# Performance work log

Measured on AMD Instinct MI355X. Metric: run time of the kernel, lower is better.

## Reference

```python
import jax, jax.numpy as jnp
import numpy as np
import math

D = 256
NS = 64
KNB = 8
VOCAB = 32000
B, S = 4, 1024
NEG = -10000.0


def _normalize(x, eps=1e-12):
    n = jnp.linalg.norm(x, axis=-1, keepdims=True)
    return x / jnp.maximum(n, eps)


def _sparsemax(z):
    # sparsemax along last axis (descending sort + cumsum threshold)
    z_sorted = -jnp.sort(-z, axis=-1)
    cumsum = jnp.cumsum(z_sorted, axis=-1)
    k = jnp.arange(1, z.shape[-1] + 1, dtype=z.dtype)
    z_check = (1.0 + k * z_sorted > cumsum).astype(z.dtype)
    k_z = z_check.sum(axis=-1, keepdims=True)
    tau = (jnp.take_along_axis(cumsum, (k_z - 1).astype(jnp.int32), axis=-1) - 1.0) / k_z
    return jnp.clip(z - tau, 0.0)


def setup_inputs() -> dict:
    key = jax.random.key(0)
    ks = jax.random.split(key, 16)
    inp = {
        'messages': jax.random.normal(ks[0], (B, S, D), jnp.float32),
        'hidden': jax.random.normal(ks[1], (B, S, D), jnp.float32),
        'x_ids': jax.random.randint(ks[2], (B, S), 0, VOCAB),
        'scn': jax.random.normal(ks[3], (B, S, NS), jnp.float32),
        'mask': jax.random.bernoulli(ks[4], 0.3, (S, S)),
        'static_nb': jax.random.randint(ks[5], (VOCAB, KNB), 0, VOCAB),
        'geo_velocity': jax.random.normal(ks[6], (B, S, NS), jnp.float32),
        'ctx_conf': jax.random.uniform(ks[7], (B, S, 1), jnp.float32),
        'current_entropy': jax.random.uniform(ks[8], (B, S), jnp.float32) * math.log(VOCAB),
        # parameters (torch Linear weight layout: [out, in])
        'W_vel': jax.random.normal(ks[9], (D, NS), jnp.float32) / np.sqrt(NS),
        'W_e1': jax.random.normal(ks[10], (8, 1), jnp.float32),
        'b_e1': jax.random.normal(ks[11], (8,), jnp.float32) * 0.1,
        'W_e2': jax.random.normal(ks[12], (1, 8), jnp.float32) / np.sqrt(8),
        'b_e2': jax.random.normal(ks[13], (1,), jnp.float32) * 0.1,
        'W_probe': jax.random.normal(ks[14], (D, D), jnp.float32) / np.sqrt(D),
        'W_gate': jnp.zeros((1, D), jnp.float32),
        'b_gate': jnp.full((1,), -4.0, jnp.float32),
    }
    return inp


def reference(messages, hidden, x_ids, scn, mask, static_nb, geo_velocity,
              ctx_conf, current_entropy, W_vel, W_e1, b_e1, W_e2, b_e2,
              W_probe, W_gate, b_gate):
    Bd, Sd, Dh = messages.shape
    f32 = messages.dtype
    blocked = (mask | jnp.eye(Sd, dtype=bool))[None]  # [1,S,S] mask + diagonal

    # ---- geo branch ----
    endpoint = _normalize(scn + 0.4 * geo_velocity)
    endpoint_sim = jnp.einsum('bsn,btn->bst', endpoint, scn)
    endpoint_sim = jnp.where(blocked, NEG, endpoint_sim)
    H_norm = jax.lax.stop_gradient(current_entropy)[..., None] / (math.log(VOCAB) + 1e-8)
    vel_h = geo_velocity @ W_vel.T
    h_aimed = _normalize(hidden + 0.3 * vel_h)
    h_msg_sim = jnp.einsum('bsd,btd->bst', h_aimed, messages)
    combined_geo = (endpoint_sim * H_norm + 0.5 * h_msg_sim) * 5.0
    combined_geo = jnp.where(blocked, NEG, combined_geo)
    ew_geo = _sparsemax(combined_geo)
    geo_agg = jnp.einsum('bst,btd->bsd', ew_geo, messages)

    # ---- static neighbor-vocab branch ----
    nb_vocab = static_nb[x_ids]  # [B,S,Knb]
    match = (x_ids[:, None, None, :] == nb_vocab[..., None]).astype(f32)  # [B,S,Knb,S]
    causal = jnp.tril(jnp.ones((Sd, Sd), f32))
    match = match * causal[None, :, None, :]
    coverage = jnp.minimum(match.sum(-1), 1.0).mean(-1, keepdims=True)  # [B,S,1]
    nb_msgs_s = jnp.einsum('bskp,bpd->bskd', match, messages)
    nb_scn_s = jnp.einsum('bskp,bpn->bskn', match, scn)
    sim_s = (nb_scn_s * scn[:, :, None, :]).sum(-1)  # [B,S,Knb]
    h_e = jax.nn.gelu(sim_s[..., None] @ W_e1.T + b_e1, approximate=False)
    edge_out = (h_e @ W_e2.T + b_e2)[..., 0]  # [B,S,Knb]
    ew_s = jax.nn.softmax(edge_out, axis=-1)
    static_agg = (nb_msgs_s * ew_s[..., None]).sum(2)

    # ---- local mode branch ----
    my_mode = jnp.argmax(scn, axis=-1)
    same_mode = (my_mode[:, :, None] == my_mode[:, None, :]).astype(f32)
    same_mode = jnp.where(blocked, 0.0, same_mode)
    scn_sim = jnp.einsum('bsn,btn->bst', scn, scn) * same_mode
    has_nb = same_mode.sum(-1, keepdims=True) > 0
    pos = jnp.arange(Sd, dtype=f32)
    pos_sim = -jnp.abs(pos[:, None] - pos[None, :])[None]
    pos_sim = jnp.where(blocked, NEG, pos_sim)
    routing_sim = jnp.where(has_nb, scn_sim, pos_sim * 0.01)
    routing_sim = jnp.where(blocked, NEG, routing_sim)
    ew_l = _sparsemax(routing_sim * 5.0)
    local_agg = jnp.einsum('bst,btd->bsd', ew_l, messages)

    # ---- gated fusion ----
    static_final = coverage * static_agg + (1.0 - coverage) * local_agg
    raw_gate = jax.nn.sigmoid(hidden @ W_gate.T + b_gate)
    geo_weight = raw_gate * ctx_conf
    agg = geo_weight * geo_agg + (1.0 - geo_weight) * static_final
    probe = _normalize(hidden @ W_probe.T)
    agg_n = _normalize(agg)
    rel = jax.nn.sigmoid((agg_n * probe).sum(-1, keepdims=True))
    return agg * rel
```

## Files before the change

### kernel.cpp

```cpp
#include <hip/hip_runtime.h>
#include <math.h>

#define D_ 256
#define NS_ 64
#define KNB_ 8
#define SEQ_ 1024
#define B_ 4
#define MAXQ_ 1024
#define NEG_ (-10000.0f)
#define BLKNEG_ (-50000.0f)

#define MSGP_B 262144
#define SCNP_B 65536
#define ASTEPS 12

typedef short bf16x8 __attribute__((ext_vector_type(8)));
typedef float f32x4 __attribute__((ext_vector_type(4)));

__device__ __forceinline__ float waveSum(float v) {
#pragma unroll
    for (int off = 32; off; off >>= 1) v += __shfl_xor(v, off, 64);
    return v;
}

__device__ __forceinline__ void waveSum2(float& a, float& b) {
#pragma unroll
    for (int off = 32; off; off >>= 1) {
        a += __shfl_xor(a, off, 64);
        b += __shfl_xor(b, off, 64);
    }
}

__device__ __forceinline__ float blockSum(float v, float* scr) {
    const int tid = threadIdx.x;
    const int wid = tid >> 6, lane = tid & 63;
    v = waveSum(v);
    __syncthreads();
    if (lane == 0) scr[wid] = v;
    __syncthreads();
    return scr[0] + scr[1] + scr[2] + scr[3];
}

__device__ __forceinline__ void blockSum4(float v[4], float (*scr4)[4]) {
    const int tid = threadIdx.x;
    const int wid = tid >> 6, lane = tid & 63;
#pragma unroll
    for (int off = 32; off; off >>= 1) {
#pragma unroll
        for (int q = 0; q < 4; ++q) v[q] += __shfl_xor(v[q], off, 64);
    }
    __syncthreads();
    if (lane == 0) {
#pragma unroll
        for (int q = 0; q < 4; ++q) scr4[wid][q] = v[q];
    }
    __syncthreads();
#pragma unroll
    for (int q = 0; q < 4; ++q)
        v[q] = scr4[0][q] + scr4[1][q] + scr4[2][q] + scr4[3][q];
}

__device__ __forceinline__ float sparsemaxTauWave(const float* zr) {
    float mx = zr[0];
#pragma unroll
    for (int i = 1; i < 16; ++i) mx = fmaxf(mx, zr[i]);
#pragma unroll
    for (int off = 32; off; off >>= 1) mx = fmaxf(mx, __shfl_xor(mx, off, 64));
    float tau = mx - 1.0f;
    for (int it = 0; it < 32; ++it) {
        float ssum = 0.f, cnt = 0.f;
#pragma unroll
        for (int i = 0; i < 16; ++i) {
            if (zr[i] > tau) { ssum += zr[i]; cnt += 1.f; }
        }
        waveSum2(ssum, cnt);
        if (cnt < 0.5f) break;
        const float nt = (ssum - 1.0f) / cnt;
        if (nt == tau) break;
        tau = nt;
    }
    return tau;
}

__device__ __forceinline__ void cvtSplit(float a, short& h, short& l) {
    const unsigned ab = __float_as_uint(a);
    h = (short)(ab >> 16);
    const float hf = __uint_as_float(ab & 0xFFFF0000u);
    l = (short)(__float_as_uint(a - hf) >> 16);
}

__device__ __forceinline__ size_t aIdx(int sg, int st, int kq, int m16, int j) {
    return ((((size_t)sg * ASTEPS + st) << 6) + (kq << 4) + m16) * 8 + j;
}

__global__ __launch_bounds__(256) void setup_kernel(
    const float* __restrict__ messages, const float* __restrict__ scn,
    const float* __restrict__ hidden, const float* __restrict__ gvel,
    const float* __restrict__ ctx, const float* __restrict__ ent,
    const float* __restrict__ W_probe, const float* __restrict__ W_vel,
    const float* __restrict__ W_gate, const float* __restrict__ b_gate,
    short* __restrict__ msgH, short* __restrict__ msgL,
    short* __restrict__ scnH, short* __restrict__ scnL,
    const unsigned int* __restrict__ maskW, int* __restrict__ flag,
    int* __restrict__ qMeta,
    short* __restrict__ wsAh, short* __restrict__ wsAl,
    float* __restrict__ wsProbe,
    int* __restrict__ wsMode, float* __restrict__ wsGw)
{
    const int bid = blockIdx.x;
    const int tid = threadIdx.x;

    if (bid < 256) {
        const int b = bid >> 6, T = bid & 63;
        const float* src = messages + (size_t)b * SEQ_ * D_;
        short* dh = msgH + (size_t)b * MSGP_B;
        short* dl = msgL + (size_t)b * MSGP_B;
#pragma unroll
        for (int it = 0; it < 2; ++it) {
            const int g = (it << 8) + tid;
            const int st = g >> 6, kq = (g >> 4) & 3, m16 = g & 15;
            const int t = (T << 4) + m16;
            const int k0 = (st << 5) + (kq << 3);
            const float4 v0 = *(const float4*)(src + (size_t)t * D_ + k0);
            const float4 v1 = *(const float4*)(src + (size_t)t * D_ + k0 + 4);
            short h[8], l[8];
            cvtSplit(v0.x, h[0], l[0]); cvtSplit(v0.y, h[1], l[1]);
            cvtSplit(v0.z, h[2], l[2]); cvtSplit(v0.w, h[3], l[3]);
            cvtSplit(v1.x, h[4], l[4]); cvtSplit(v1.y, h[5], l[5]);
            cvtSplit(v1.z, h[6], l[6]); cvtSplit(v1.w, h[7], l[7]);
            const size_t o = (((size_t)T * 8 + st) << 9) + (size_t)((kq << 4) + m16) * 8;
            *(short4*)(dh + o) = make_short4(h[0], h[1], h[2], h[3]);
            *(short4*)(dh + o + 4) = make_short4(h[4], h[5], h[6], h[7]);
            *(short4*)(dl + o) = make_short4(l[0], l[1], l[2], l[3]);
            *(short4*)(dl + o + 4) = make_short4(l[4], l[5], l[6], l[7]);
        }
        return;
    }

    if (bid < 320) {
        const int i = bid - 256;
        const int b = i >> 4;
        const float* src = scn + (size_t)b * SEQ_ * NS_;
        short* dh = scnH + (size_t)b * SCNP_B;
        short* dl = scnL + (size_t)b * SCNP_B;
#pragma unroll
        for (int tt = 0; tt < 4; ++tt) {
            const int T = ((i & 15) << 2) + tt;
            if (tid < 128) {
                const int st = tid >> 6, kq = (tid >> 4) & 3, m16 = tid & 15;
                const int t = (T << 4) + m16;
                const int k0 = (st << 5) + (kq << 3);
                const float4 v0 = *(const float4*)(src + (size_t)t * NS_ + k0);
                const float4 v1 = *(const float4*)(src + (size_t)t * NS_ + k0 + 4);
                short h[8], l[8];
                cvtSplit(v0.x, h[0], l[0]); cvtSplit(v0.y, h[1], l[1]);
                cvtSplit(v0.z, h[2], l[2]); cvtSplit(v0.w, h[3], l[3]);
                cvtSplit(v1.x, h[4], l[4]); cvtSplit(v1.y, h[5], l[5]);
                cvtSplit(v1.z, h[6], l[6]); cvtSplit(v1.w, h[7], l[7]);
                const size_t o = (((size_t)T * 2 + st) << 9) + (size_t)((kq << 4) + m16) * 8;
                *(short4*)(dh + o) = make_short4(h[0], h[1], h[2], h[3]);
                *(short4*)(dh + o + 4) = make_short4(h[4], h[5], h[6], h[7]);
                *(short4*)(dl + o) = make_short4(l[0], l[1], l[2], l[3]);
                *(short4*)(dl + o + 4) = make_short4(l[4], l[5], l[6], l[7]);
            }
        }
        return;
    }

    if (bid == 320) {
        __shared__ int notI, notF;
        if (tid == 0) { notI = 0; notF = 0; qMeta[0] = 0; qMeta[1] = 0; }
        __syncthreads();
        int ni = 0, nf = 0;
        for (int i = tid; i < 1024; i += 256) {
            const unsigned int w = maskW[i];
            if (w != 0u && w != 1u) ni = 1;
            if (w != 0u && w != 0x3f800000u) nf = 1;
        }
        if (ni) atomicOr(&notI, 1);
        if (nf) atomicOr(&notF, 1);
        __syncthreads();
        if (tid == 0) *flag = (!notI) ? 0 : ((!notF) ? 2 : 1);
        return;
    }

    __shared__ float scr4[4][4];
    const int rowBase = (bid - 321) << 3;
    const int wid = tid >> 6, lane = tid & 63;
    const float* h0 = hidden + (size_t)rowBase * D_;

    float vh[8] = {};
    for (int e = 0; e < NS_; e += 4) {
        const float4 wv4 = *(const float4*)(W_vel + (size_t)tid * NS_ + e);
#pragma unroll
        for (int r = 0; r < 8; ++r) {
            const float4 g4 = *(const float4*)(gvel + (size_t)(rowBase + r) * NS_ + e);
            vh[r] = fmaf(g4.x, wv4.x, fmaf(g4.y, wv4.y, fmaf(g4.z, wv4.z, fmaf(g4.w, wv4.w, vh[r]))));
        }
    }
    float pr[8] = {};
    for (int e = 0; e < D_; e += 4) {
        const float4 wp4 = *(const float4*)(W_probe + (size_t)tid * D_ + e);
#pragma unroll
        for (int r = 0; r < 8; ++r) {
            const float4 h4 = *(const float4*)(h0 + (size_t)r * D_ + e);
            pr[r] = fmaf(h4.x, wp4.x, fmaf(h4.y, wp4.y, fmaf(h4.z, wp4.z, fmaf(h4.w, wp4.w, pr[r]))));
        }
    }

#pragma unroll
    for (int rr = 0; rr < 2; ++rr) {
        const int r = (wid << 1) + rr, row = rowBase + r;
        const int sg = row >> 4, m16 = row & 15;
        const float sv = scn[(size_t)row * NS_ + lane];
        const float gv = gvel[(size_t)row * NS_ + lane];
        const float Hn = ent[row] / 10.373491191781864f;
        const float e = sv + 0.4f * gv;
        const float ss = waveSum(e * e);
        const int stE = lane >> 5, kqE = (lane & 31) >> 3, jE = lane & 7;
        short hh, ll;
        cvtSplit((e / fmaxf(sqrtf(ss), 1e-12f)) * 5.0f * Hn, hh, ll);
        wsAh[aIdx(sg, stE, kqE, m16, jE)] = hh;
        wsAl[aIdx(sg, stE, kqE, m16, jE)] = ll;
        cvtSplit(5.0f * sv, hh, ll);
        wsAh[aIdx(sg, 2 + stE, kqE, m16, jE)] = hh;
        wsAl[aIdx(sg, 2 + stE, kqE, m16, jE)] = ll;
        float v = sv; int idx = lane;
#pragma unroll
        for (int off = 1; off < 64; off <<= 1) {
            const float ov = __shfl_xor(v, off, 64);
            const int   oi = __shfl_xor(idx, off, 64);
            if (ov > v || (ov == v && oi < idx)) { v = ov; idx = oi; }
        }
        float gd = 0.f;
#pragma unroll
        for (int j = 0; j < 4; ++j) {
            const int d = lane + (j << 6);
            gd = fmaf(h0[(size_t)r * D_ + d], W_gate[d], gd);
        }
        gd = waveSum(gd);
        if (lane == 0) {
            wsMode[row] = idx;
            const float raw = 1.f / (1.f + expf(-(gd + b_gate[0])));
            wsGw[row] = raw * ctx[row];
        }
    }

    const int stH = 4 + (tid >> 5), kqH = (tid & 31) >> 3, jH = tid & 7;
#pragma unroll
    for (int g = 0; g < 2; ++g) {
        float ha4[4], va[4], vp[4];
#pragma unroll
        for (int q = 0; q < 4; ++q) {
            const int r = (g << 2) + q;
            ha4[q] = h0[(size_t)r * D_ + tid] + 0.3f * vh[r];
            va[q] = ha4[q] * ha4[q];
            vp[q] = pr[(g << 2) + q] * pr[(g << 2) + q];
        }
        blockSum4(va, scr4);
        blockSum4(vp, scr4);
#pragma unroll
        for (int q = 0; q < 4; ++q) {
            const int r = (g << 2) + q;
            const int row = rowBase + r;
            const int sg = row >> 4, m16 = row & 15;
            short hh, ll;
            cvtSplit((ha4[q] / fmaxf(sqrtf(va[q]), 1e-12f)) * 2.5f, hh, ll);
            wsAh[aIdx(sg, stH, kqH, m16, jH)] = hh;
            wsAl[aIdx(sg, stH, kqH, m16, jH)] = ll;
            wsProbe[(size_t)row * D_ + tid] = pr[r] / fmaxf(sqrtf(vp[q]), 1e-12f);
        }
    }
}

__global__ __launch_bounds__(512) void sims_kernel(
    const short* __restrict__ msgH, const short* __restrict__ msgL,
    const short* __restrict__ scnH, const short* __restrict__ scnL,
    const short* __restrict__ wsAh, const short* __restrict__ wsAl,
    const int* __restrict__ wsMode,
    const void* __restrict__ maskP,
    const int* __restrict__ maskFlag,
    float* __restrict__ zgO,
    float* __restrict__ zlO)
{
    const int bid = blockIdx.x;
    const int half = bid & 1;
    const int sg = (bid >> 1) & 63;
    const int b = bid >> 7;
    const int sBase = sg << 4;
    const int rowBase = (b << 10) + sBase;
    const int tid = threadIdx.x;
    const int w = tid >> 6, l = tid & 63;
    const int m16 = l & 15, kq = l >> 4;
    const int l8 = l << 3;

    const int sgA = (b << 6) + sg;
    const short* AhB = wsAh + (size_t)sgA * (ASTEPS * 512) + l8;
    const short* AlB = wsAl + (size_t)sgA * (ASTEPS * 512) + l8;

    f32x4 accG[4], accL8[4];
#pragma unroll
    for (int ct = 0; ct < 4; ++ct) {
        accG[ct] = (f32x4){0.f, 0.f, 0.f, 0.f};
        accL8[ct] = (f32x4){0.f, 0.f, 0.f, 0.f};
    }

#pragma unroll
    for (int st = 0; st < 2; ++st) {
        const bf16x8 aeh = *(const bf16x8*)(AhB + (st << 9));
        const bf16x8 ael = *(const bf16x8*)(AlB + (st << 9));
        const bf16x8 ash = *(const bf16x8*)(AhB + ((2 + st) << 9));
        const bf16x8 asl = *(const bf16x8*)(AlB + ((2 + st) << 9));
#pragma unroll
        for (int ct = 0; ct < 4; ++ct) {
            const int mtile = (half << 5) + (w << 2) + ct;
            const size_t bo = (size_t)b * SCNP_B + (((size_t)mtile * 2 + st) << 9) + l8;
            const bf16x8 bh = *(const bf16x8*)(scnH + bo);
            const bf16x8 bl = *(const bf16x8*)(scnL + bo);
            accG[ct] = __builtin_amdgcn_mfma_f32_16x16x32_bf16(aeh, bh, accG[ct], 0, 0, 0);
            accG[ct] = __builtin_amdgcn_mfma_f32_16x16x32_bf16(aeh, bl, accG[ct], 0, 0, 0);
            accG[ct] = __builtin_amdgcn_mfma_f32_16x16x32_bf16(ael, bh, accG[ct], 0, 0, 0);
            accL8[ct] = __builtin_amdgcn_mfma_f32_16x16x32_bf16(ash, bh, accL8[ct], 0, 0, 0);
            accL8[ct] = __builtin_amdgcn_mfma_f32_16x16x32_bf16(ash, bl, accL8[ct], 0, 0, 0);
            accL8[ct] = __builtin_amdgcn_mfma_f32_16x16x32_bf16(asl, bh, accL8[ct], 0, 0, 0);
        }
    }
#pragma unroll
    for (int st = 0; st < 8; ++st) {
        const bf16x8 ah = *(const bf16x8*)(AhB + ((4 + st) << 9));
        const bf16x8 al = *(const bf16x8*)(AlB + ((4 + st) << 9));
#pragma unroll
        for (int ct = 0; ct < 4; ++ct) {
            const int mtile = (half << 5) + (w << 2) + ct;
            const size_t bo = (size_t)b * MSGP_B + (((size_t)mtile * 8 + st) << 9) + l8;
            const bf16x8 bh = *(const bf16x8*)(msgH + bo);
            const bf16x8 bl = *(const bf16x8*)(msgL + bo);
            accG[ct] = __builtin_amdgcn_mfma_f32_16x16x32_bf16(ah, bh, accG[ct], 0, 0, 0);
            accG[ct] = __builtin_amdgcn_mfma_f32_16x16x32_bf16(ah, bl, accG[ct], 0, 0, 0);
            accG[ct] = __builtin_amdgcn_mfma_f32_16x16x32_bf16(al, bh, accG[ct], 0, 0, 0);
        }
    }

    const int tBase = (half << 9) + (w << 6);
    const int mf = *maskFlag;
    const int4 mS4 = *(const int4*)(wsMode + rowBase + (kq << 2));
    const int mSq[4] = {mS4.x, mS4.y, mS4.z, mS4.w};
#pragma unroll
    for (int ct = 0; ct < 4; ++ct) {
        const int t = tBase + (ct << 4) + m16;
        const int mdt = wsMode[(b << 10) + t];
#pragma unroll
        for (int q = 0; q < 4; ++q) {
            const int r = (kq << 2) + q;
            const int s_r = sBase + r;
            const size_t mb = (size_t)s_r * SEQ_ + t;
            int blk;
            if (mf == 1)      blk = ((const unsigned char*)maskP)[mb] != 0;
            else if (mf == 2) blk = ((const float*)maskP)[mb] != 0.f;
            else              blk = ((const int*)maskP)[mb] != 0;
            if (s_r == t) blk = 1;
            zgO[(size_t)(rowBase + r) * SEQ_ + t] = blk ? NEG_ : accG[ct][q];
            const int sm = (!blk) && (mdt == mSq[q]);
            zlO[(size_t)(rowBase + r) * SEQ_ + t] =
                blk ? BLKNEG_ : (sm ? accL8[ct][q] : 0.0f);
        }
    }
}

__global__ __launch_bounds__(256) void route4_kernel(
    const float* __restrict__ messages,
    const float* __restrict__ scn,
    const int* __restrict__ x_ids,
    const int* __restrict__ static_nb,
    const float* __restrict__ W_e1,
    const float* __restrict__ b_e1,
    const float* __restrict__ W_e2,
    const float* __restrict__ b_e2,
    const float* __restrict__ wsProbe,
    const float* __restrict__ wsGw,
    const float* __restrict__ zgA,
    const float* __restrict__ zlA,
    float* __restrict__ wq,
    int* __restrict__ qRows,
    int* __restrict__ qMeta,
    float* __restrict__ out)
{
    __shared__ uint2 lst[4][256];
    __shared__ float ewLds[4][8];
    __shared__ int   mlist[4][64];

    const int jb = blockIdx.x;
    const int tid = threadIdx.x;
    const int wid = tid >> 6, lane = tid & 63;
    const int base = jb << 1;
    const int row = (wid == 0) ? base
                  : (wid == 1) ? base + 1
                  : (wid == 2) ? 4094 - base
                               : 4095 - base;
    const int b = row >> 10, s_r = row & 1023;
    const float* msgB = messages + (size_t)b * SEQ_ * D_;
    const float* scnB = scn + (size_t)b * SEQ_ * NS_;
    const unsigned long long ltmask = (1ull << lane) - 1ull;
    const int d4 = lane << 2;

    float zrG[16], zrL[16];
    {
        const float4* zgp = (const float4*)(zgA + (size_t)row * SEQ_ + (lane << 4));
        const float4* zlp = (const float4*)(zlA + (size_t)row * SEQ_ + (lane << 4));
#pragma unroll
        for (int q = 0; q < 4; ++q) {
            const float4 g4 = zgp[q];
            zrG[q * 4 + 0] = g4.x; zrG[q * 4 + 1] = g4.y;
            zrG[q * 4 + 2] = g4.z; zrG[q * 4 + 3] = g4.w;
            const float4 l4 = zlp[q];
            zrL[q * 4 + 0] = l4.x; zrL[q * 4 + 1] = l4.y;
            zrL[q * 4 + 2] = l4.z; zrL[q * 4 + 3] = l4.w;
        }
    }

    const int q = x_ids[row];
    int nb[KNB_];
#pragma unroll
    for (int k = 0; k < KNB_; ++k) nb[k] = static_nb[(size_t)q * KNB_ + k];
    const float ss_l = scnB[(size_t)s_r * NS_ + lane];
    float simk[KNB_] = {};
    unsigned matchedMask = 0;
    int mcW = 0;
    const int* xb = x_ids + (b << 10);
    for (int pb = 0; pb <= s_r; pb += 64) {
        const int p = pb + lane;
        const int id = (p <= s_r) ? xb[p] : -2147483647;
        unsigned kmask = 0;
#pragma unroll
        for (int k = 0; k < KNB_; ++k) kmask |= (id == nb[k]) ? (1u << k) : 0u;
        unsigned long long mb = __ballot(kmask != 0u);
        while (mb) {
            const int src = __ffsll(mb) - 1; mb &= mb - 1;
            const unsigned kms = (unsigned)__shfl((int)kmask, src, 64);
            const int pp = pb + src;
            float pv = scnB[(size_t)pp * NS_ + lane] * ss_l;
            pv = waveSum(pv);
            matchedMask |= kms;
#pragma unroll
            for (int k = 0; k < KNB_; ++k) {
                if ((kms >> k) & 1u) {
                    simk[k] += pv;
                    if (mcW < 64) { if (lane == 0) mlist[wid][mcW] = (pp << 3) | k; ++mcW; }
                }
            }
        }
    }
    const int kk = lane >> 3, jjn = lane & 7;
    float sv = simk[0];
#pragma unroll
    for (int k = 1; k < KNB_; ++k) sv = (kk == k) ? simk[k] : sv;
    const float xx = sv * W_e1[jjn] + b_e1[jjn];
    float eo = 0.5f * xx * (1.f + erff(xx * 0.70710678118654752f)) * W_e2[jjn];
    eo += __shfl_xor(eo, 1, 64); eo += __shfl_xor(eo, 2, 64); eo += __shfl_xor(eo, 4, 64);
    eo += b_e2[0];
    float m2 = eo;
    m2 = fmaxf(m2, __shfl_xor(m2, 8, 64));
    m2 = fmaxf(m2, __shfl_xor(m2, 16, 64));
    m2 = fmaxf(m2, __shfl_xor(m2, 32, 64));
    const float exv = expf(eo - m2);
    float smv = exv;
    smv += __shfl_xor(smv, 8, 64); smv += __shfl_xor(smv, 16, 64); smv += __shfl_xor(smv, 32, 64);
    if ((lane & 7) == 0) ewLds[wid][kk] = exv / smv;

    const float cov = (float)__popc(matchedMask) * 0.125f;
    const float gw = wsGw[row];
    const float coefG = gw;
    const float coefL = (1.f - gw) * (1.f - cov);
    const float coefS = (1.f - gw) * cov;

    int fl = 0;
#pragma unroll
    for (int j = 0; j < 16; ++j) fl |= (zrL[j] != 0.0f && zrL[j] > -40000.f);
    const int hasNb = __any(fl);
    if (!hasNb) {
#pragma unroll
        for (int j = 0; j < 16; ++j) {
            const int t = (lane << 4) + j;
            zrL[j] = (zrL[j] <= -40000.f) ? BLKNEG_ : -0.05f * fabsf((float)(s_r - t));
        }
    }

    const float tauG = sparsemaxTauWave(zrG);
    int supG = 0;
#pragma unroll
    for (int j = 0; j < 16; ++j) supG += __popcll(__ballot(zrG[j] > tauG));
    const float tauL = sparsemaxTauWave(zrL);
    int supL = 0;
#pragma unroll
    for (int j = 0; j < 16; ++j) supL += __popcll(__ballot(zrL[j] > tauL));
    const bool gDense = supG > 96;
    const bool lDense = supL > 96;

    int cnt = 0;
    if (!gDense) {
#pragma unroll
        for (int j = 0; j < 16; ++j) {
            const float wv = zrG[j] - tauG;
            const bool take = wv > 0.f;
            const unsigned long long m = __ballot(take);
            if (take) {
                const int pos = cnt + __popcll(m & ltmask);
                lst[wid][pos] = make_uint2((unsigned)((lane << 4) + j),
                                           __float_as_uint(coefG * wv));
            }
            cnt += __popcll(m);
        }
    }
    if (!lDense) {
#pragma unroll
        for (int j = 0; j < 16; ++j) {
            const float wv = zrL[j] - tauL;
            const bool take = wv > 0.f;
            const unsigned long long m = __ballot(take);
            if (take) {
                const int pos = cnt + __popcll(m & ltmask);
                lst[wid][pos] = make_uint2((unsigned)((lane << 4) + j),
                                           __float_as_uint(coefL * wv));
            }
            cnt += __popcll(m);
        }
    }
    const int nm = (mcW < 64) ? mcW : 64;
    for (int i = lane; i < nm; i += 64) {
        const int ee = mlist[wid][i];
        lst[wid][cnt + i] = make_uint2((unsigned)(ee >> 3),
                                       __float_as_uint(coefS * ewLds[wid][ee & 7]));
    }
    cnt += nm;

    float ox = 0.f, oy = 0.f, oz2 = 0.f, ow = 0.f;
    int i = 0;
    for (; i + 4 <= cnt; i += 4) {
        const uint2 e0 = lst[wid][i + 0];
        const uint2 e1 = lst[wid][i + 1];
        const uint2 e2 = lst[wid][i + 2];
        const uint2 e3 = lst[wid][i + 3];
        const float4 m0 = *(const float4*)(msgB + (size_t)e0.x * D_ + d4);
        const float4 m1 = *(const float4*)(msgB + (size_t)e1.x * D_ + d4);
        const float4 m2b = *(const float4*)(msgB + (size_t)e2.x * D_ + d4);
        const float4 m3 = *(const float4*)(msgB + (size_t)e3.x * D_ + d4);
        const float w0 = __uint_as_float(e0.y), w1 = __uint_as_float(e1.y);
        const float w2 = __uint_as_float(e2.y), w3 = __uint_as_float(e3.y);
        ox = fmaf(w0, m0.x, fmaf(w1, m1.x, fmaf(w2, m2b.x, fmaf(w3, m3.x, ox))));
        oy = fmaf(w0, m0.y, fmaf(w1, m1.y, fmaf(w2, m2b.y, fmaf(w3, m3.y, oy))));
        oz2 = fmaf(w0, m0.z, fmaf(w1, m1.z, fmaf(w2, m2b.z, fmaf(w3, m3.z, oz2))));
        ow = fmaf(w0, m0.w, fmaf(w1, m1.w, fmaf(w2, m2b.w, fmaf(w3, m3.w, ow))));
    }
    for (; i < cnt; ++i) {
        const uint2 e0 = lst[wid][i];
        const float w0 = __uint_as_float(e0.y);
        const float4 m0 = *(const float4*)(msgB + (size_t)e0.x * D_ + d4);
        ox = fmaf(w0, m0.x, ox); oy = fmaf(w0, m0.y, oy);
        oz2 = fmaf(w0, m0.z, oz2); ow = fmaf(w0, m0.w, ow);
    }

    int slot = -1;
    if (gDense || lDense) {
        int s0 = 0;
        if (lane == 0) s0 = atomicAdd(&qMeta[0], 1);
        slot = __shfl(s0, 0, 64);
    }
    if (slot >= 0 && slot < MAXQ_) {
#pragma unroll
        for (int qd = 0; qd < 4; ++qd) {
            float4 w4;
            float* wv4 = &w4.x;
#pragma unroll
            for (int u = 0; u < 4; ++u) {
                const int j = qd * 4 + u;
                float w = 0.f;
                if (gDense) w += coefG * fmaxf(zrG[j] - tauG, 0.f);
                if (lDense) w += coefL * fmaxf(zrL[j] - tauL, 0.f);
                wv4[u] = w;
            }
            *(float4*)(wq + (size_t)slot * SEQ_ + (lane << 4) + qd * 4) = w4;
        }
        if (lane == 0) qRows[slot] = row;
        *(float4*)(out + (size_t)row * D_ + d4) = make_float4(ox, oy, oz2, ow);
        return;
    }
    if (slot >= MAXQ_) {
#pragma unroll
        for (int j = 0; j < 16; ++j) {
            float wv = 0.f;
            if (gDense) wv += coefG * fmaxf(zrG[j] - tauG, 0.f);
            if (lDense) wv += coefL * fmaxf(zrL[j] - tauL, 0.f);
            unsigned long long m = __ballot(wv > 0.f);
            while (m) {
                const int s0 = __ffsll(m) - 1; m &= m - 1;
                const float w0 = __shfl(wv, s0, 64);
                const float4 m4 = *(const float4*)(msgB + (size_t)((s0 << 4) + j) * D_ + d4);
                ox = fmaf(w0, m4.x, ox); oy = fmaf(w0, m4.y, oy);
                oz2 = fmaf(w0, m4.z, oz2); ow = fmaf(w0, m4.w, ow);
            }
        }
    }

    float ssq = ox * ox + oy * oy + oz2 * oz2 + ow * ow;
    ssq = waveSum(ssq);
    const float nrm = fmaxf(sqrtf(ssq), 1e-12f);
    const float4 pr = *(const float4*)(wsProbe + (size_t)row * D_ + d4);
    float dp = (ox * pr.x + oy * pr.y + oz2 * pr.z + ow * pr.w) / nrm;
    dp = waveSum(dp);
    const float rel = 1.f / (1.f + expf(-dp));
    *(float4*)(out + (size_t)row * D_ + d4) =
        make_float4(ox * rel, oy * rel, oz2 * rel, ow * rel);
}

__global__ __launch_bounds__(256) void cleanup_kernel(
    const float* __restrict__ messages,
    const float* __restrict__ wsProbe,
    const float* __restrict__ wq,
    const int* __restrict__ qRows,
    int* __restrict__ qMeta,
    float* __restrict__ out)
{
    __shared__ float wsh[SEQ_];
    __shared__ float scr[4];
    __shared__ int idxSh;
    const int tid = threadIdx.x;
    const int nq = (qMeta[0] < MAXQ_) ? qMeta[0] : MAXQ_;
    for (;;) {
        __syncthreads();
        if (tid == 0) idxSh = atomicAdd(&qMeta[1], 1);
        __syncthreads();
        const int idx = idxSh;
        if (idx >= nq) break;
        const int row = qRows[idx];
        const int b = row >> 10;
        const float* msgB = messages + (size_t)b * SEQ_ * D_;
        for (int i = tid; i < SEQ_; i += 256)
            wsh[i] = wq[(size_t)idx * SEQ_ + i];
        __syncthreads();
        float acc = out[(size_t)row * D_ + tid];
        for (int t = 0; t < SEQ_; t += 4) {
            acc = fmaf(wsh[t + 0], msgB[(size_t)(t + 0) * D_ + tid],
                  fmaf(wsh[t + 1], msgB[(size_t)(t + 1) * D_ + tid],
                  fmaf(wsh[t + 2], msgB[(size_t)(t + 2) * D_ + tid],
                  fmaf(wsh[t + 3], msgB[(size_t)(t + 3) * D_ + tid], acc))));
        }
        const float ssq = blockSum(acc * acc, scr);
        const float nrm = fmaxf(sqrtf(ssq), 1e-12f);
        const float dp = blockSum((acc / nrm) * wsProbe[(size_t)row * D_ + tid], scr);
        const float rel = 1.f / (1.f + expf(-dp));
        out[(size_t)row * D_ + tid] = acc * rel;
    }
}

extern "C" void kernel_launch(void* const* d_in, const int* in_sizes, int n_in,
                              void* d_out, int out_size, void* d_ws, size_t ws_size,
                              hipStream_t stream) {
    const float* messages  = (const float*)d_in[0];
    const float* hidden    = (const float*)d_in[1];
    const int*   x_ids     = (const int*)d_in[2];
    const float* scn       = (const float*)d_in[3];
    const void*  mask      = d_in[4];
    const int*   static_nb = (const int*)d_in[5];
    const float* gvel      = (const float*)d_in[6];
    const float* ctx       = (const float*)d_in[7];
    const float* ent       = (const float*)d_in[8];
    const float* W_vel     = (const float*)d_in[9];
    const float* W_e1      = (const float*)d_in[10];
    const float* b_e1      = (const float*)d_in[11];
    const float* W_e2      = (const float*)d_in[12];
    const float* b_e2      = (const float*)d_in[13];
    const float* W_probe   = (const float*)d_in[14];
    const float* W_gate    = (const float*)d_in[15];
    const float* b_gate    = (const float*)d_in[16];
    float* out = (float*)d_out;
    (void)in_sizes; (void)n_in; (void)out_size; (void)ws_size;

    char* ws = (char*)d_ws;
    size_t o = 0;
    int* flag      = (int*)(ws + o);   o += 256;
    short* wsAh    = (short*)(ws + o); o += (size_t)B_ * SEQ_ * 384 * 2;
    short* wsAl    = (short*)(ws + o); o += (size_t)B_ * SEQ_ * 384 * 2;
    float* wsProbe = (float*)(ws + o); o += (size_t)B_ * SEQ_ * D_ * 4;
    int* wsMode    = (int*)(ws + o);   o += (size_t)B_ * SEQ_ * 4;
    float* wsGw    = (float*)(ws + o); o += (size_t)B_ * SEQ_ * 4;
    short* msgH    = (short*)(ws + o); o += (size_t)B_ * MSGP_B * 2;
    short* msgL    = (short*)(ws + o); o += (size_t)B_ * MSGP_B * 2;
    short* scnH    = (short*)(ws + o); o += (size_t)B_ * SCNP_B * 2;
    short* scnL    = (short*)(ws + o); o += (size_t)B_ * SCNP_B * 2;
    float* zgW     = (float*)(ws + o); o += (size_t)B_ * SEQ_ * SEQ_ * 4;
    float* zlW     = (float*)(ws + o); o += (size_t)B_ * SEQ_ * SEQ_ * 4;
    int* qMeta     = (int*)(ws + o);   o += 256;
    int* qRows     = (int*)(ws + o);   o += (size_t)MAXQ_ * 4;
    float* wq      = (float*)msgH;

    setup_kernel<<<dim3(833), dim3(256), 0, stream>>>(
        messages, scn, hidden, gvel, ctx, ent, W_probe, W_vel, W_gate, b_gate,
        msgH, msgL, scnH, scnL, (const unsigned int*)mask, flag, qMeta,
        wsAh, wsAl, wsProbe, wsMode, wsGw);
    sims_kernel<<<dim3(512), dim3(512), 0, stream>>>(
        msgH, msgL, scnH, scnL, wsAh, wsAl, wsMode, mask, flag, zgW, zlW);
    route4_kernel<<<dim3(B_ * SEQ_ / 4), dim3(256), 0, stream>>>(
        messages, scn, x_ids, static_nb, W_e1, b_e1, W_e2, b_e2,
        wsProbe, wsGw, zgW, zlW, wq, qRows, qMeta, out);
    cleanup_kernel<<<dim3(64), dim3(256), 0, stream>>>(
        messages, wsProbe, wq, qRows, qMeta, out);
}
```

Baseline: 111.2 us.

## Retile sims kernel to 32x256 blocks and fuse the two sparsemax tau solves

The sims kernel now gives each block 32 query rows by 256 key columns instead of 16 rows by 512 columns. Each B fragment loaded from global memory is reused across two A row-tiles, which halves B traffic per MFMA, at the cost of more accumulator registers. In route4, the separate iterative sparsemax threshold solves for the G and L branches are merged into one loop with interleaved reductions. This shares the loop and shuffle latency, but the loop now runs until both branches converge, and a zero count is handled by clamping instead of an early break.

```diff
diff --git a/kernel.cpp b/kernel.cpp
--- a/kernel.cpp
+++ b/kernel.cpp
@@ -23,14 +23,6 @@
     return v;
 }
 
-__device__ __forceinline__ void waveSum2(float& a, float& b) {
-#pragma unroll
-    for (int off = 32; off; off >>= 1) {
-        a += __shfl_xor(a, off, 64);
-        b += __shfl_xor(b, off, 64);
-    }
-}
-
 __device__ __forceinline__ float blockSum(float v, float* scr) {
     const int tid = threadIdx.x;
     const int wid = tid >> 6, lane = tid & 63;
@@ -58,28 +50,6 @@
 #pragma unroll
     for (int q = 0; q < 4; ++q)
         v[q] = scr4[0][q] + scr4[1][q] + scr4[2][q] + scr4[3][q];
-}
-
-__device__ __forceinline__ float sparsemaxTauWave(const float* zr) {
-    float mx = zr[0];
-#pragma unroll
-    for (int i = 1; i < 16; ++i) mx = fmaxf(mx, zr[i]);
-#pragma unroll
-    for (int off = 32; off; off >>= 1) mx = fmaxf(mx, __shfl_xor(mx, off, 64));
-    float tau = mx - 1.0f;
-    for (int it = 0; it < 32; ++it) {
-        float ssum = 0.f, cnt = 0.f;
-#pragma unroll
-        for (int i = 0; i < 16; ++i) {
-            if (zr[i] > tau) { ssum += zr[i]; cnt += 1.f; }
-        }
-        waveSum2(ssum, cnt);
-        if (cnt < 0.5f) break;
-        const float nt = (ssum - 1.0f) / cnt;
-        if (nt == tau) break;
-        tau = nt;
-    }
-    return tau;
 }
 
 __device__ __forceinline__ void cvtSplit(float a, short& h, short& l) {
@@ -284,85 +254,108 @@
     float* __restrict__ zlO)
 {
     const int bid = blockIdx.x;
-    const int half = bid & 1;
-    const int sg = (bid >> 1) & 63;
     const int b = bid >> 7;
-    const int sBase = sg << 4;
+    const int rem = bid & 127;
+    const int rg = rem >> 2;
+    const int qt = rem & 3;
+    const int sBase = rg << 5;
     const int rowBase = (b << 10) + sBase;
     const int tid = threadIdx.x;
     const int w = tid >> 6, l = tid & 63;
     const int m16 = l & 15, kq = l >> 4;
     const int l8 = l << 3;
 
-    const int sgA = (b << 6) + sg;
-    const short* AhB = wsAh + (size_t)sgA * (ASTEPS * 512) + l8;
-    const short* AlB = wsAl + (size_t)sgA * (ASTEPS * 512) + l8;
-
-    f32x4 accG[4], accL8[4];
-#pragma unroll
-    for (int ct = 0; ct < 4; ++ct) {
-        accG[ct] = (f32x4){0.f, 0.f, 0.f, 0.f};
-        accL8[ct] = (f32x4){0.f, 0.f, 0.f, 0.f};
-    }
+    const int sgA = (b << 6) + (rg << 1);
+    const short* Ah0 = wsAh + (size_t)sgA * (ASTEPS * 512) + l8;
+    const short* Al0 = wsAl + (size_t)sgA * (ASTEPS * 512) + l8;
+    const short* Ah1 = Ah0 + ASTEPS * 512;
+    const short* Al1 = Al0 + ASTEPS * 512;
+
+    f32x4 accG[2][2], accL8[2][2];
+#pragma unroll
+    for (int mA = 0; mA < 2; ++mA)
+#pragma unroll
+        for (int ct = 0; ct < 2; ++ct) {
+            accG[mA][ct] = (f32x4){0.f, 0.f, 0.f, 0.f};
+            accL8[mA][ct] = (f32x4){0.f, 0.f, 0.f, 0.f};
+        }
 
 #pragma unroll
     for (int st = 0; st < 2; ++st) {
-        const bf16x8 aeh = *(const bf16x8*)(AhB + (st << 9));
-        const bf16x8 ael = *(const bf16x8*)(AlB + (st << 9));
-        const bf16x8 ash = *(const bf16x8*)(AhB + ((2 + st) << 9));
-        const bf16x8 asl = *(const bf16x8*)(AlB + ((2 + st) << 9));
-#pragma unroll
-        for (int ct = 0; ct < 4; ++ct) {
-            const int mtile = (half << 5) + (w << 2) + ct;
+        const bf16x8 aeh0 = *(const bf16x8*)(Ah0 + (st << 9));
+        const bf16x8 ael0 = *(const bf16x8*)(Al0 + (st << 9));
+        const bf16x8 ash0 = *(const bf16x8*)(Ah0 + ((2 + st) << 9));
+        const bf16x8 asl0 = *(const bf16x8*)(Al0 + ((2 + st) << 9));
+        const bf16x8 aeh1 = *(const bf16x8*)(Ah1 + (st << 9));
+        const bf16x8 ael1 = *(const bf16x8*)(Al1 + (st << 9));
+        const bf16x8 ash1 = *(const bf16x8*)(Ah1 + ((2 + st) << 9));
+        const bf16x8 asl1 = *(const bf16x8*)(Al1 + ((2 + st) << 9));
+#pragma unroll
+        for (int ct = 0; ct < 2; ++ct) {
+            const int mtile = (qt << 4) + (w << 1) + ct;
             const size_t bo = (size_t)b * SCNP_B + (((size_t)mtile * 2 + st) << 9) + l8;
             const bf16x8 bh = *(const bf16x8*)(scnH + bo);
             const bf16x8 bl = *(const bf16x8*)(scnL + bo);
-            accG[ct] = __builtin_amdgcn_mfma_f32_16x16x32_bf16(aeh, bh, accG[ct], 0, 0, 0);
-            accG[ct] = __builtin_amdgcn_mfma_f32_16x16x32_bf16(aeh, bl, accG[ct], 0, 0, 0);
-            accG[ct] = __builtin_amdgcn_mfma_f32_16x16x32_bf16(ael, bh, accG[ct], 0, 0, 0);
-            accL8[ct] = __builtin_amdgcn_mfma_f32_16x16x32_bf16(ash, bh, accL8[ct], 0, 0, 0);
-            accL8[ct] = __builtin_amdgcn_mfma_f32_16x16x32_bf16(ash, bl, accL8[ct], 0, 0, 0);
-            accL8[ct] = __builtin_amdgcn_mfma_f32_16x16x32_bf16(asl, bh, accL8[ct], 0, 0, 0);
+            accG[0][ct] = __builtin_amdgcn_mfma_f32_16x16x32_bf16(aeh0, bh, accG[0][ct], 0, 0, 0);
+            accG[0][ct] = __builtin_amdgcn_mfma_f32_16x16x32_bf16(aeh0, bl, accG[0][ct], 0, 0, 0);
+            accG[0][ct] = __builtin_amdgcn_mfma_f32_16x16x32_bf16(ael0, bh, accG[0][ct], 0, 0, 0);
+            accL8[0][ct] = __builtin_amdgcn_mfma_f32_16x16x32_bf16(ash0, bh, accL8[0][ct], 0, 0, 0);
+            accL8[0][ct] = __builtin_amdgcn_mfma_f32_16x16x32_bf16(ash0, bl, accL8[0][ct], 0, 0, 0);
+            accL8[0][ct] = __builtin_amdgcn_mfma_f32_16x16x32_bf16(asl0, bh, accL8[0][ct], 0, 0, 0);
+            accG[1][ct] = __builtin_amdgcn_mfma_f32_16x16x32_bf16(aeh1, bh, accG[1][ct], 0, 0, 0);
+            accG[1][ct] = __builtin_amdgcn_mfma_f32_16x16x32_bf16(aeh1, bl, accG[1][ct], 0, 0, 0);
+            accG[1][ct] = __builtin_amdgcn_mfma_f32_16x16x32_bf16(ael1, bh, accG[1][ct], 0, 0, 0);
+            accL8[1][ct] = __builtin_amdgcn_mfma_f32_16x16x32_bf16(ash1, bh, accL8[1][ct], 0, 0, 0);
+            accL8[1][ct] = __builtin_amdgcn_mfma_f32_16x16x32_bf16(ash1, bl, accL8[1][ct], 0, 0, 0);
+            accL8[1][ct] = __builtin_amdgcn_mfma_f32_16x16x32_bf16(asl1, bh, accL8[1][ct], 0, 0, 0);
         }
     }
 #pragma unroll
     for (int st = 0; st < 8; ++st) {
-        const bf16x8 ah = *(const bf16x8*)(AhB + ((4 + st) << 9));
-        const bf16x8 al = *(const bf16x8*)(AlB + ((4 + st) << 9));
-#pragma unroll
-        for (int ct = 0; ct < 4; ++ct) {
-            const int mtile = (half << 5) + (w << 2) + ct;
+        const bf16x8 ah0 = *(const bf16x8*)(Ah0 + ((4 + st) << 9));
+        const bf16x8 al0 = *(const bf16x8*)(Al0 + ((4 + st) << 9));
+        const bf16x8 ah1 = *(const bf16x8*)(Ah1 + ((4 + st) << 9));
+        const bf16x8 al1 = *(const bf16x8*)(Al1 + ((4 + st) << 9));
+#pragma unroll
+        for (int ct = 0; ct < 2; ++ct) {
+            const int mtile = (qt << 4) + (w << 1) + ct;
             const size_t bo = (size_t)b * MSGP_B + (((size_t)mtile * 8 + st) << 9) + l8;
             const bf16x8 bh = *(const bf16x8*)(msgH + bo);
             const bf16x8 bl = *(const bf16x8*)(msgL + bo);
-            accG[ct] = __builtin_amdgcn_mfma_f32_16x16x32_bf16(ah, bh, accG[ct], 0, 0, 0);
-            accG[ct] = __builtin_amdgcn_mfma_f32_16x16x32_bf16(ah, bl, accG[ct], 0, 0, 0);
-            accG[ct] = __builtin_amdgcn_mfma_f32_16x16x32_bf16(al, bh, accG[ct], 0, 0, 0);
-        }
-    }
-
-    const int tBase = (half << 9) + (w << 6);
+            accG[0][ct] = __builtin_amdgcn_mfma_f32_16x16x32_bf16(ah0, bh, accG[0][ct], 0, 0, 0);
+            accG[0][ct] = __builtin_amdgcn_mfma_f32_16x16x32_bf16(ah0, bl, accG[0][ct], 0, 0, 0);
+            accG[0][ct] = __builtin_amdgcn_mfma_f32_16x16x32_bf16(al0, bh, accG[0][ct], 0, 0, 0);
+            accG[1][ct] = __builtin_amdgcn_mfma_f32_16x16x32_bf16(ah1, bh, accG[1][ct], 0, 0, 0);
+            accG[1][ct] = __builtin_amdgcn_mfma_f32_16x16x32_bf16(ah1, bl, accG[1][ct], 0, 0, 0);
+            accG[1][ct] = __builtin_amdgcn_mfma_f32_16x16x32_bf16(al1, bh, accG[1][ct], 0, 0, 0);
+        }
+    }
+
+    const int tBase = (qt << 8) + (w << 5);
     const int mf = *maskFlag;
-    const int4 mS4 = *(const int4*)(wsMode + rowBase + (kq << 2));
-    const int mSq[4] = {mS4.x, mS4.y, mS4.z, mS4.w};
-#pragma unroll
-    for (int ct = 0; ct < 4; ++ct) {
-        const int t = tBase + (ct << 4) + m16;
-        const int mdt = wsMode[(b << 10) + t];
-#pragma unroll
-        for (int q = 0; q < 4; ++q) {
-            const int r = (kq << 2) + q;
-            const int s_r = sBase + r;
-            const size_t mb = (size_t)s_r * SEQ_ + t;
-            int blk;
-            if (mf == 1)      blk = ((const unsigned char*)maskP)[mb] != 0;
-            else if (mf == 2) blk = ((const float*)maskP)[mb] != 0.f;
-            else              blk = ((const int*)maskP)[mb] != 0;
-            if (s_r == t) blk = 1;
-            zgO[(size_t)(rowBase + r) * SEQ_ + t] = blk ? NEG_ : accG[ct][q];
-            const int sm = (!blk) && (mdt == mSq[q]);
-            zlO[(size_t)(rowBase + r) * SEQ_ + t] =
-                blk ? BLKNEG_ : (sm ? accL8[ct][q] : 0.0f);
+#pragma unroll
+    for (int mA = 0; mA < 2; ++mA) {
+        const int4 mS4 = *(const int4*)(wsMode + rowBase + (mA << 4) + (kq << 2));
+        const int mSq[4] = {mS4.x, mS4.y, mS4.z, mS4.w};
+#pragma unroll
+        for (int ct = 0; ct < 2; ++ct) {
+            const int t = tBase + (ct << 4) + m16;
+            const int mdt = wsMode[(b << 10) + t];
+#pragma unroll
+            for (int q = 0; q < 4; ++q) {
+                const int r = (mA << 4) + (kq << 2) + q;
+                const int s_r = sBase + r;
+                const size_t mb = (size_t)s_r * SEQ_ + t;
+                int blk;
+                if (mf == 1)      blk = ((const unsigned char*)maskP)[mb] != 0;
+                else if (mf == 2) blk = ((const float*)maskP)[mb] != 0.f;
+                else              blk = ((const int*)maskP)[mb] != 0;
+                if (s_r == t) blk = 1;
+                zgO[(size_t)(rowBase + r) * SEQ_ + t] = blk ? NEG_ : accG[mA][ct][q];
+                const int sm = (!blk) && (mdt == mSq[q]);
+                zlO[(size_t)(rowBase + r) * SEQ_ + t] =
+                    blk ? BLKNEG_ : (sm ? accL8[mA][ct][q] : 0.0f);
+            }
         }
     }
 }
@@ -485,14 +478,39 @@
         }
     }
 
-    const float tauG = sparsemaxTauWave(zrG);
-    int supG = 0;
-#pragma unroll
-    for (int j = 0; j < 16; ++j) supG += __popcll(__ballot(zrG[j] > tauG));
-    const float tauL = sparsemaxTauWave(zrL);
-    int supL = 0;
-#pragma unroll
-    for (int j = 0; j < 16; ++j) supL += __popcll(__ballot(zrL[j] > tauL));
+    float mxG = zrG[0], mxL = zrL[0];
+#pragma unroll
+    for (int j = 1; j < 16; ++j) { mxG = fmaxf(mxG, zrG[j]); mxL = fmaxf(mxL, zrL[j]); }
+#pragma unroll
+    for (int off = 32; off; off >>= 1) {
+        mxG = fmaxf(mxG, __shfl_xor(mxG, off, 64));
+        mxL = fmaxf(mxL, __shfl_xor(mxL, off, 64));
+    }
+    float tauG = mxG - 1.f, tauL = mxL - 1.f;
+    for (int it = 0; it < 32; ++it) {
+        float sG = 0.f, cG = 0.f, sL = 0.f, cL = 0.f;
+#pragma unroll
+        for (int j = 0; j < 16; ++j) {
+            if (zrG[j] > tauG) { sG += zrG[j]; cG += 1.f; }
+            if (zrL[j] > tauL) { sL += zrL[j]; cL += 1.f; }
+        }
+#pragma unroll
+        for (int off = 32; off; off >>= 1) {
+            sG += __shfl_xor(sG, off, 64); cG += __shfl_xor(cG, off, 64);
+            sL += __shfl_xor(sL, off, 64); cL += __shfl_xor(cL, off, 64);
+        }
+        const float nG = (sG - 1.f) / fmaxf(cG, 1.f);
+        const float nL = (sL - 1.f) / fmaxf(cL, 1.f);
+        if (nG == tauG && nL == tauL) break;
+        tauG = nG; tauL = nL;
+    }
+
+    int supG = 0, supL = 0;
+#pragma unroll
+    for (int j = 0; j < 16; ++j) {
+        supG += __popcll(__ballot(zrG[j] > tauG));
+        supL += __popcll(__ballot(zrL[j] > tauL));
+    }
     const bool gDense = supG > 96;
     const bool lDense = supL > 96;
 
```

New measurement: 105.3 us. 5.2% less time.
